# Kernel tuning notes

Hardware: AMD Instinct MI355X
Metric: run time of the kernel (lower is better)

## Reference

```python
import jax, jax.numpy as jnp
import numpy as np

N = 8192   # nodes per modality
D = 128    # hidden_channels
H = 2      # transformer heads
R = 15     # relations in HeteroConv (use_speaker='no')
E = 16384  # edges per relation
L = 2      # num_layers
# relation src/dst node-type ids: 0=audio, 1=text, 2=visual (dict order: a/v/t past, a/v/t future, a/v/t self, then cross)
SRC = np.array([0, 2, 1, 0, 2, 1, 0, 2, 1, 0, 0, 2, 2, 1, 1])
DST = np.array([0, 2, 1, 0, 2, 1, 0, 2, 1, 2, 1, 0, 1, 0, 2])


def setup_inputs() -> dict:
    key = jax.random.key(0)
    ks = jax.random.split(key, 18)
    f = lambda k, sh: jax.random.normal(k, sh, dtype=jnp.float32) * 0.05
    return {
        "x_audio": jax.random.normal(ks[0], (N, D), jnp.float32),
        "x_text": jax.random.normal(ks[1], (N, D), jnp.float32),
        "x_visual": jax.random.normal(ks[2], (N, D), jnp.float32),
        "edge_index": jax.random.randint(ks[3], (R, 2, E), 0, N, jnp.int32),
        "Wrel": f(ks[4], (L, R, D, D)),
        "brel": f(ks[5], (L, R, D)),
        "Wroot": f(ks[6], (L, R, D, D)),
        "Wq": f(ks[7], (D, H * D)), "bq": f(ks[8], (H * D,)),
        "Wk": f(ks[9], (D, H * D)), "bk": f(ks[10], (H * D,)),
        "Wv": f(ks[11], (D, H * D)), "bv": f(ks[12], (H * D,)),
        "Wskip": f(ks[13], (D, D)), "bskip": f(ks[14], (D,)),
        "gamma": jnp.ones((D,), jnp.float32),
        "beta": jnp.zeros((D,), jnp.float32),
    }


def reference(x_audio, x_text, x_visual, edge_index, Wrel, brel, Wroot,
              Wq, bq, Wk, bk, Wv, bv, Wskip, bskip, gamma, beta):
    src_t = jnp.asarray(SRC)
    dst_t = jnp.asarray(DST)
    x = jnp.stack([x_audio, x_text, x_visual])           # [3, N, D]
    src_idx = edge_index[:, 0]                            # [R, E]
    dst_idx = edge_index[:, 1]                            # [R, E]
    rel = jnp.arange(R)

    # --- HeteroConv of 15 GraphConvs (aggr='add' inside, 'mean' over the 5 relations per dst type) ---
    seg = (rel[:, None] * N + dst_idx).reshape(-1)        # per-relation segment ids
    for l in range(L):
        feats = jnp.take_along_axis(x[src_t], src_idx[:, :, None], axis=1)     # [R, E, D]
        msg = jax.ops.segment_sum(feats.reshape(R * E, D), seg,
                                  num_segments=R * N).reshape(R, N, D)          # scatter-add per relation
        out = (jnp.einsum('rnd,rde->rne', msg, Wrel[l]) + brel[l][:, None, :]
               + jnp.einsum('rnd,rde->rne', x[dst_t], Wroot[l]))                # lin_rel(agg) + lin_root(x_dst)
        x = jax.nn.relu(jnp.zeros_like(x).at[dst_t].add(out) / 5.0)            # mean over 5 relations per dst

    # --- hetero_to_homo: concat audio, text, visual (offsets 0, N, 2N) ---
    hx = x.reshape(3 * N, D)
    src_h = (src_t[:, None] * N + src_idx).reshape(-1)    # [R*E]
    dst_h = (dst_t[:, None] * N + dst_idx).reshape(-1)

    # --- TransformerConv (concat=False -> head mean, root skip) ---
    q = (hx @ Wq + bq).reshape(3 * N, H, D)
    k = (hx @ Wk + bk).reshape(3 * N, H, D)
    v = (hx @ Wv + bv).reshape(3 * N, H, D)
    logits = jnp.einsum('ehd,ehd->eh', q[dst_h], k[src_h]) / jnp.sqrt(jnp.float32(D))
    m = jax.ops.segment_max(logits, dst_h, num_segments=3 * N)
    p = jnp.exp(logits - m[dst_h])
    denom = jax.ops.segment_sum(p, dst_h, num_segments=3 * N)
    alpha = p / denom[dst_h]                              # segment softmax over incoming edges
    agg = jax.ops.segment_sum(alpha[:, :, None] * v[src_h], dst_h, num_segments=3 * N)  # [3N, H, D]
    out = agg.mean(axis=1) + hx @ Wskip + bskip

    # --- BatchNorm1d (training-mode batch stats) + leaky_relu ---
    mu = out.mean(axis=0)
    var = ((out - mu) ** 2).mean(axis=0)
    y = (out - mu) / jnp.sqrt(var + 1e-5) * gamma + beta
    y = jax.nn.leaky_relu(y)                              # negative_slope=0.01 (torch default)
    return y.reshape(3, N, D)                             # [audio, text, visual]
```

## Files before the change

kernel.cpp:

```cpp
#include <hip/hip_runtime.h>
#include <hip/hip_bf16.h>

#define NN 8192
#define DD 128
#define HH 2
#define RR 15
#define EE 16384
#define NLAYER 2
#define NMOD 3
#define TN (NMOD*NN)
#define NE (RR*EE)
#define NB (TN*5)
#define SCB (NB/256)

#define SRC_BITS 0x16818618u
#define DST_BITS 0x21198618u
__device__ __forceinline__ int srcOf(int r) { return (SRC_BITS >> (2 * r)) & 3; }
__device__ __forceinline__ int dstOf(int r) { return (DST_BITS >> (2 * r)) & 3; }

typedef __attribute__((ext_vector_type(8))) short bf16x8;
typedef __attribute__((ext_vector_type(4))) float f32x4;
typedef _Float16 h2 __attribute__((ext_vector_type(2)));

__device__ __forceinline__ unsigned short f2bf(float v) {
    union { float f; unsigned int u; } x; x.f = v;
    unsigned int r = (x.u + 0x7fffu + ((x.u >> 16) & 1u)) >> 16;
    return (unsigned short)r;
}
__device__ __forceinline__ float bf2f(unsigned int bits16) {
    return __uint_as_float(bits16 << 16);
}

__device__ __forceinline__ float dot8_f16(uint4 a, uint4 b, float acc) {
#if __has_builtin(__builtin_amdgcn_fdot2)
    acc = __builtin_amdgcn_fdot2(__builtin_bit_cast(h2, a.x), __builtin_bit_cast(h2, b.x), acc, false);
    acc = __builtin_amdgcn_fdot2(__builtin_bit_cast(h2, a.y), __builtin_bit_cast(h2, b.y), acc, false);
    acc = __builtin_amdgcn_fdot2(__builtin_bit_cast(h2, a.z), __builtin_bit_cast(h2, b.z), acc, false);
    acc = __builtin_amdgcn_fdot2(__builtin_bit_cast(h2, a.w), __builtin_bit_cast(h2, b.w), acc, false);
#else
    h2 av, bv;
    av = __builtin_bit_cast(h2, a.x); bv = __builtin_bit_cast(h2, b.x);
    acc += (float)av.x * (float)bv.x + (float)av.y * (float)bv.y;
    av = __builtin_bit_cast(h2, a.y); bv = __builtin_bit_cast(h2, b.y);
    acc += (float)av.x * (float)bv.x + (float)av.y * (float)bv.y;
    av = __builtin_bit_cast(h2, a.z); bv = __builtin_bit_cast(h2, b.z);
    acc += (float)av.x * (float)bv.x + (float)av.y * (float)bv.y;
    av = __builtin_bit_cast(h2, a.w); bv = __builtin_bit_cast(h2, b.w);
    acc += (float)av.x * (float)bv.x + (float)av.y * (float)bv.y;
#endif
    return acc;
}

__device__ __forceinline__ h2 h2shfl_xor(h2 a, int off) {
    return __builtin_bit_cast(h2, __shfl_xor(__builtin_bit_cast(int, a), off));
}

__global__ __launch_bounds__(256) void prep_all(
        const float* __restrict__ Wrel, const float* __restrict__ Wroot,
        const float* __restrict__ brel,
        const float* __restrict__ Wq, const float* __restrict__ Wk,
        const float* __restrict__ Wv, const float* __restrict__ Wskip,
        const float* __restrict__ xa, const float* __restrict__ xt,
        const float* __restrict__ xv,
        unsigned short* __restrict__ WcatT, float* __restrict__ bsum,
        unsigned short* __restrict__ WqT, unsigned short* __restrict__ WkT,
        unsigned short* __restrict__ WvT, unsigned short* __restrict__ WskipT,
        unsigned short* __restrict__ xb, int* __restrict__ cnt) {
    int y = blockIdx.y;
    int t = blockIdx.x * 256 + threadIdx.x;
    if (y < 36) {
        int mat = y / 6, j = y - mat * 6;
        int l = mat / 3, m = mat - l * 3;
        int k = t >> 7, oc = t & 127;
        unsigned short* W = WcatT + (size_t)mat * 128 * 768;
        if (j < 5) {
            int r = 3 * j;
            while (((DST_BITS >> (2 * r)) & 3) != (unsigned)m) r++;
            W[(size_t)oc * 768 + j * 128 + k] = f2bf(Wrel[(size_t)(l * RR + r) * 16384 + t]);
        } else {
            float s = 0.f;
            #pragma unroll
            for (int r = 0; r < RR; r++)
                if (((DST_BITS >> (2 * r)) & 3) == (unsigned)m) s += Wroot[(size_t)(l * RR + r) * 16384 + t];
            W[(size_t)oc * 768 + 640 + k] = f2bf(s);
            if (blockIdx.x == 0 && threadIdx.x < 128) {
                float b = 0.f;
                #pragma unroll
                for (int r = 0; r < RR; r++)
                    if (((DST_BITS >> (2 * r)) & 3) == (unsigned)m) b += brel[(l * RR + r) * 128 + threadIdx.x];
                bsum[mat * 128 + threadIdx.x] = b;
            }
        }
    } else if (y < 39) {
        int which = y - 36;
        const float* s = which == 0 ? Wq : which == 1 ? Wk : Wv;
        unsigned short* d = which == 0 ? WqT : which == 1 ? WkT : WvT;
        #pragma unroll
        for (int it = 0; it < 2; it++) {
            int tt = t + it * 16384;
            int k = tt >> 8, c = tt & 255;
            d[c * 128 + k] = f2bf(s[tt]);
        }
    } else if (y == 39) {
        int k = t >> 7, c = t & 127;
        WskipT[c * 128 + k] = f2bf(Wskip[t]);
    } else if (y == 40) {
        for (int i = t; i < NB + 256; i += 16384) cnt[i] = 0;
    } else {
        int m = y - 41;
        const float* s = m == 0 ? xa : m == 1 ? xt : xv;
        unsigned short* d = xb + (size_t)m * NN * DD;
        for (int i = t * 4; i < NN * DD; i += 16384 * 4) {
            float4 v = *(const float4*)(s + i);
            uint2 o;
            o.x = (unsigned)f2bf(v.x) | ((unsigned)f2bf(v.y) << 16);
            o.y = (unsigned)f2bf(v.z) | ((unsigned)f2bf(v.w) << 16);
            *(uint2*)(d + i) = o;
        }
    }
}

__global__ void count_edges(const int* __restrict__ edge, int* __restrict__ cnt) {
    int t = blockIdx.x * 256 + threadIdx.x;
    if (t >= NE) return;
    int r = t >> 14, e = t & (EE - 1);
    int dst = edge[r * 2 * EE + EE + e];
    atomicAdd(&cnt[(dstOf(r) * NN + dst) * 5 + r / 3], 1);
}

__global__ __launch_bounds__(256) void scan_reduce(const int* __restrict__ cnt,
                                                   int* __restrict__ part) {
    int t = threadIdx.x;
    int v = cnt[blockIdx.x * 256 + t];
    #pragma unroll
    for (int off = 32; off >= 1; off >>= 1) v += __shfl_xor(v, off);
    __shared__ int ws[4];
    if ((t & 63) == 0) ws[t >> 6] = v;
    __syncthreads();
    if (t == 0) part[blockIdx.x] = ws[0] + ws[1] + ws[2] + ws[3];
}

__global__ __launch_bounds__(512) void scan_mid(int* __restrict__ part, int* __restrict__ bs) {
    __shared__ int lds[512];
    int t = threadIdx.x;
    int v = (t < SCB) ? part[t] : 0;
    lds[t] = v;
    __syncthreads();
    for (int off = 1; off < 512; off <<= 1) {
        int u = (t >= off) ? lds[t - off] : 0;
        __syncthreads();
        lds[t] += u;
        __syncthreads();
    }
    if (t < SCB) part[t] = lds[t] - v;
    if (t == 0) bs[NB] = NE;
}

__global__ __launch_bounds__(256) void scan_final(const int* __restrict__ cnt,
                                                  const int* __restrict__ part,
                                                  int* __restrict__ bs,
                                                  int* __restrict__ cursor) {
    int t = threadIdx.x;
    int lane = t & 63, w = t >> 6;
    int i = blockIdx.x * 256 + t;
    int v = cnt[i];
    int inc = v;
    #pragma unroll
    for (int off = 1; off < 64; off <<= 1) {
        int u = __shfl_up(inc, off);
        if (lane >= off) inc += u;
    }
    __shared__ int wtot[4];
    if (lane == 63) wtot[w] = inc;
    __syncthreads();
    int wofs = 0;
    #pragma unroll
    for (int j = 0; j < 4; j++) if (j < w) wofs += wtot[j];
    int ex = part[blockIdx.x] + wofs + inc - v;
    bs[i] = ex;
    cursor[i] = ex;
}

__global__ void place_edges(const int* __restrict__ edge, int* __restrict__ cursor,
                            unsigned int* __restrict__ sorted) {
    int t = blockIdx.x * 256 + threadIdx.x;
    if (t >= NE) return;
    int r = t >> 14, e = t & (EE - 1);
    int src = edge[r * 2 * EE + e];
    int dst = edge[r * 2 * EE + EE + e];
    int pos = atomicAdd(&cursor[(dstOf(r) * NN + dst) * 5 + r / 3], 1);
    sorted[pos] = (unsigned int)(srcOf(r) * NN + src);
}

__global__ __launch_bounds__(256) void gather_msg(const unsigned short* __restrict__ x,
                                                  const unsigned int* __restrict__ sorted,
                                                  const int* __restrict__ bs,
                                                  unsigned short* __restrict__ msg) {
    int h = blockIdx.x * 4 + (threadIdx.x >> 6);
    int lane = threadIdx.x & 63;
    const unsigned int* x32 = (const unsigned int*)x;
    unsigned int* mrow = (unsigned int*)(msg + (size_t)h * 768);
    int base = h * 5;
    int st = bs[base];
    #pragma unroll
    for (int j = 0; j < 5; j++) {
        int nx = bs[base + j + 1];
        float a0 = 0.f, a1 = 0.f;
        for (int e = st; e < nx; e++) {
            unsigned int u = x32[(size_t)sorted[e] * 64 + lane];
            a0 += bf2f(u & 0xffffu);
            a1 += bf2f(u >> 16);
        }
        mrow[j * 64 + lane] = (unsigned)f2bf(a0) | ((unsigned)f2bf(a1) << 16);
        st = nx;
    }
    mrow[320 + lane] = x32[(size_t)h * 64 + lane];
}

__global__ __launch_bounds__(256) void layer_gemm(const unsigned short* __restrict__ msg,
                                                  const unsigned short* __restrict__ WcatT_l,
                                                  const float* __restrict__ bsum_l,
                                                  unsigned short* __restrict__ xnxt) {
    __shared__ unsigned short lds[24576];
    unsigned short* Alds = lds;
    unsigned short* Blds = lds + 8192;
    const int m = blockIdx.y;
    const int row0 = blockIdx.x * 64;
    const unsigned short* A = msg + ((size_t)m * NN + row0) * 768;
    const unsigned short* BT = WcatT_l + (size_t)m * 128 * 768;
    const int tid = threadIdx.x, lane = tid & 63, w = tid >> 6;
    const int lr = lane & 15, lk = lane >> 4;
    f32x4 acc[8];
    #pragma unroll
    for (int nj = 0; nj < 8; nj++) acc[nj] = (f32x4){0.f, 0.f, 0.f, 0.f};
    #pragma unroll 1
    for (int kc = 0; kc < 6; kc++) {
        __syncthreads();
        #pragma unroll
        for (int i = 0; i < 4; i++) {
            int c = i * 256 + tid;
            int row = c >> 4, k0 = (c & 15) << 3;
            uint4 va = *(const uint4*)(A + (size_t)row * 768 + kc * 128 + k0);
            *(uint4*)((char*)Alds + ((row * 256 + k0 * 2) ^ ((row & 7) << 4))) = va;
        }
        #pragma unroll
        for (int i = 0; i < 8; i++) {
            int c = i * 256 + tid;
            int row = c >> 4, k0 = (c & 15) << 3;
            uint4 vb = *(const uint4*)(BT + (size_t)row * 768 + kc * 128 + k0);
            *(uint4*)((char*)Blds + ((row * 256 + k0 * 2) ^ ((row & 7) << 4))) = vb;
        }
        __syncthreads();
        #pragma unroll
        for (int ks = 0; ks < 4; ks++) {
            int arow = w * 16 + lr;
            bf16x8 a = *(const bf16x8*)((char*)Alds + ((arow * 256 + (ks * 32 + lk * 8) * 2) ^ ((arow & 7) << 4)));
            bf16x8 b[8];
            #pragma unroll
            for (int nj = 0; nj < 8; nj++) {
                int brow = nj * 16 + lr;
                b[nj] = *(const bf16x8*)((char*)Blds + ((brow * 256 + (ks * 32 + lk * 8) * 2) ^ ((brow & 7) << 4)));
            }
            #pragma unroll
            for (int nj = 0; nj < 8; nj++)
                acc[nj] = __builtin_amdgcn_mfma_f32_16x16x32_bf16(a, b[nj], acc[nj], 0, 0, 0);
        }
    }
    __syncthreads();
    float* Clds = (float*)lds;
    #pragma unroll
    for (int nj = 0; nj < 8; nj++) {
        int col = nj * 16 + lr;
        float bb = bsum_l[m * 128 + col];
        #pragma unroll
        for (int r = 0; r < 4; r++) {
            int row = w * 16 + lk * 4 + r;
            float v = (acc[nj][r] + bb) * 0.2f;
            Clds[row * 128 + col] = v > 0.f ? v : 0.f;
        }
    }
    __syncthreads();
    unsigned short* X = xnxt + ((size_t)m * NN + row0) * 128;
    #pragma unroll
    for (int i = 0; i < 4; i++) {
        int c = i * 256 + tid;
        int row = c >> 4, c0 = (c & 15) * 8;
        float4 fa = *(const float4*)(Clds + row * 128 + c0);
        float4 fb = *(const float4*)(Clds + row * 128 + c0 + 4);
        uint4 pk;
        pk.x = (unsigned)f2bf(fa.x) | ((unsigned)f2bf(fa.y) << 16);
        pk.y = (unsigned)f2bf(fa.z) | ((unsigned)f2bf(fa.w) << 16);
        pk.z = (unsigned)f2bf(fb.x) | ((unsigned)f2bf(fb.y) << 16);
        pk.w = (unsigned)f2bf(fb.z) | ((unsigned)f2bf(fb.w) << 16);
        *(uint4*)(X + (size_t)row * 128 + c0) = pk;
    }
}

template<int MODE>
__device__ __forceinline__ void gemm_tile(const unsigned short* __restrict__ A,
                                          const unsigned short* __restrict__ BT,
                                          const float* __restrict__ bias,
                                          void* __restrict__ Cout,
                                          int ldc, int colofs, int row0,
                                          unsigned short* lds, float oscale = 1.f) {
    unsigned short* Alds = lds;
    unsigned short* Blds = lds + 16384;
    const int tid = threadIdx.x;
    const int lane = tid & 63;
    const int w = tid >> 6;
    #pragma unroll
    for (int i = 0; i < 8; i++) {
        int c = i * 256 + tid;
        int row = c >> 4;
        int k0 = (c & 15) << 3;
        uint4 va = *(const uint4*)(A + (size_t)(row0 + row) * 128 + k0);
        *(uint4*)((char*)Alds + (((row * 256 + k0 * 2)) ^ ((row & 7) << 4))) = va;
        uint4 vb = *(const uint4*)(BT + (size_t)row * 128 + k0);
        *(uint4*)((char*)Blds + (((row * 256 + k0 * 2)) ^ ((row & 7) << 4))) = vb;
    }
    __syncthreads();
    f32x4 acc[2][8];
    #pragma unroll
    for (int mi = 0; mi < 2; mi++)
        #pragma unroll
        for (int nj = 0; nj < 8; nj++) acc[mi][nj] = (f32x4){0.f, 0.f, 0.f, 0.f};
    const int lr = lane & 15, lk = lane >> 4;
    #pragma unroll
    for (int ks = 0; ks < 4; ks++) {
        bf16x8 a[2], b[8];
        #pragma unroll
        for (int mi = 0; mi < 2; mi++) {
            int row = w * 32 + mi * 16 + lr;
            a[mi] = *(const bf16x8*)((char*)Alds + ((row * 256 + (ks * 32 + lk * 8) * 2) ^ ((row & 7) << 4)));
        }
        #pragma unroll
        for (int nj = 0; nj < 8; nj++) {
            int row = nj * 16 + lr;
            b[nj] = *(const bf16x8*)((char*)Blds + ((row * 256 + (ks * 32 + lk * 8) * 2) ^ ((row & 7) << 4)));
        }
        #pragma unroll
        for (int mi = 0; mi < 2; mi++)
            #pragma unroll
            for (int nj = 0; nj < 8; nj++)
                acc[mi][nj] = __builtin_amdgcn_mfma_f32_16x16x32_bf16(a[mi], b[nj], acc[mi][nj], 0, 0, 0);
    }
    __syncthreads();
    float* Clds = (float*)lds;
    #pragma unroll
    for (int mi = 0; mi < 2; mi++) {
        #pragma unroll
        for (int nj = 0; nj < 8; nj++) {
            int ccl = nj * 16 + lr;
            float bb = bias ? bias[ccl] : 0.f;
            #pragma unroll
            for (int r = 0; r < 4; r++) {
                int row = w * 32 + mi * 16 + lk * 4 + r;
                Clds[row * 128 + ccl] = acc[mi][nj][r] + bb;
            }
        }
    }
    __syncthreads();
    #pragma unroll
    for (int p = 0; p < 8; p++) {
        int row = p * 16 + (tid >> 4);
        int c0 = (tid & 15) * 8;
        float4 fa = *(const float4*)(Clds + row * 128 + c0);
        float4 fb = *(const float4*)(Clds + row * 128 + c0 + 4);
        if (MODE == 3) {
            unsigned r0 = __builtin_bit_cast(unsigned, __builtin_amdgcn_cvt_pkrtz(fa.x * oscale, fa.y * oscale));
            unsigned r1 = __builtin_bit_cast(unsigned, __builtin_amdgcn_cvt_pkrtz(fa.z * oscale, fa.w * oscale));
            unsigned r2 = __builtin_bit_cast(unsigned, __builtin_amdgcn_cvt_pkrtz(fb.x * oscale, fb.y * oscale));
            unsigned r3 = __builtin_bit_cast(unsigned, __builtin_amdgcn_cvt_pkrtz(fb.z * oscale, fb.w * oscale));
            uint4 pk = {r0, r1, r2, r3};
            *(uint4*)((unsigned short*)Cout + (size_t)(row0 + row) * ldc + colofs + c0) = pk;
        } else {
            float* Cf = (float*)Cout;
            *(float4*)(Cf + (size_t)(row0 + row) * ldc + colofs + c0) = fa;
            *(float4*)(Cf + (size_t)(row0 + row) * ldc + colofs + c0 + 4) = fb;
        }
    }
}

__global__ __launch_bounds__(256) void qkvskip_gemm(const unsigned short* __restrict__ xbf,
                                                    const unsigned short* __restrict__ WqT,
                                                    const unsigned short* __restrict__ WkT,
                                                    const unsigned short* __restrict__ WvT,
                                                    const unsigned short* __restrict__ WskipT,
                                                    const float* __restrict__ bq,
                                                    const float* __restrict__ bk,
                                                    const float* __restrict__ bv,
                                                    const float* __restrict__ bskip,
                                                    unsigned short* __restrict__ qb,
                                                    unsigned short* __restrict__ kb,
                                                    unsigned short* __restrict__ vb,
                                                    float* __restrict__ out) {
    __shared__ unsigned short lds[2 * 16384];
    int y = blockIdx.y;
    if (y < 6) {
        int which = y >> 1, half = y & 1;
        const unsigned short* BT = (which == 0 ? WqT : which == 1 ? WkT : WvT) + half * 16384;
        const float* bias = (which == 0 ? bq : which == 1 ? bk : bv) + half * 128;
        unsigned short* C = (which == 0 ? qb : which == 1 ? kb : vb);
        float os = (which == 0) ? 0.08838834764831845f : 1.f;
        gemm_tile<3>(xbf, BT, bias, C, 256, half * 128, blockIdx.x * 128, lds, os);
    } else {
        gemm_tile<0>(xbf, WskipT, bskip, out, 128, 0, blockIdx.x * 128, lds);
    }
}

__global__ __launch_bounds__(256) void attn_fused(const unsigned short* __restrict__ qb,
                                                  const unsigned short* __restrict__ kb,
                                                  const unsigned short* __restrict__ vb,
                                                  const unsigned int* __restrict__ sorted,
                                                  const int* __restrict__ bs,
                                                  float* __restrict__ out) {
    int node = blockIdx.x * 4 + (threadIdx.x >> 6);
    int lane = threadIdx.x & 63;
    int g = lane >> 4, p = lane & 15;
    uint4 q0 = *(const uint4*)(qb + (size_t)node * 256 + p * 8);
    uint4 q1 = *(const uint4*)(qb + (size_t)node * 256 + 128 + p * 8);
    float s0 = 0.f, s1 = 0.f;
    h2 a0h[4], a1h[4];
    #pragma unroll
    for (int jj = 0; jj < 4; jj++) { a0h[jj] = (h2){0, 0}; a1h[jj] = (h2){0, 0}; }
    int st = bs[node * 5], en = bs[node * 5 + 5];
    int idx = st + g;
    unsigned int vcur = (idx < en) ? sorted[idx] : 0u;
    for (int base = st; base < en; base += 4) {
        unsigned int vnext = (idx + 4 < en) ? sorted[idx + 4] : 0u;
        bool valid = idx < en;
        const unsigned short* krow = kb + (size_t)vcur * 256;
        const unsigned short* vrow = vb + (size_t)vcur * 256;
        uint4 k0r = *(const uint4*)(krow + p * 8);
        uint4 k1r = *(const uint4*)(krow + 128 + p * 8);
        uint4 v0r = *(const uint4*)(vrow + p * 8);
        uint4 v1r = *(const uint4*)(vrow + 128 + p * 8);
        float d0 = dot8_f16(q0, k0r, 0.f);
        float d1 = dot8_f16(q1, k1r, 0.f);
        #pragma unroll
        for (int off = 8; off >= 1; off >>= 1) {
            d0 += __shfl_xor(d0, off);
            d1 += __shfl_xor(d1, off);
        }
        float p0 = valid ? __expf(d0) : 0.f;
        float p1 = valid ? __expf(d1) : 0.f;
        s0 += p0; s1 += p1;
        h2 ph0 = (h2){(_Float16)p0, (_Float16)p0};
        h2 ph1 = (h2){(_Float16)p1, (_Float16)p1};
        a0h[0] += ph0 * __builtin_bit_cast(h2, v0r.x);
        a0h[1] += ph0 * __builtin_bit_cast(h2, v0r.y);
        a0h[2] += ph0 * __builtin_bit_cast(h2, v0r.z);
        a0h[3] += ph0 * __builtin_bit_cast(h2, v0r.w);
        a1h[0] += ph1 * __builtin_bit_cast(h2, v1r.x);
        a1h[1] += ph1 * __builtin_bit_cast(h2, v1r.y);
        a1h[2] += ph1 * __builtin_bit_cast(h2, v1r.z);
        a1h[3] += ph1 * __builtin_bit_cast(h2, v1r.w);
        vcur = vnext;
        idx += 4;
    }
    #pragma unroll
    for (int off = 32; off >= 16; off >>= 1) {
        s0 += __shfl_xor(s0, off);
        s1 += __shfl_xor(s1, off);
        #pragma unroll
        for (int jj = 0; jj < 4; jj++) {
            a0h[jj] += h2shfl_xor(a0h[jj], off);
            a1h[jj] += h2shfl_xor(a1h[jj], off);
        }
    }
    if (g == 0) {
        float inv0 = (s0 > 0.f) ? 0.5f / s0 : 0.f;
        float inv1 = (s1 > 0.f) ? 0.5f / s1 : 0.f;
        float a0[8], a1[8];
        #pragma unroll
        for (int jj = 0; jj < 4; jj++) {
            a0[2 * jj] = (float)a0h[jj].x; a0[2 * jj + 1] = (float)a0h[jj].y;
            a1[2 * jj] = (float)a1h[jj].x; a1[2 * jj + 1] = (float)a1h[jj].y;
        }
        float* op = out + (size_t)node * 128 + p * 8;
        float4 ska = *(const float4*)op;
        float4 skb = *(const float4*)(op + 4);
        float4 ra, rb;
        ra.x = a0[0] * inv0 + a1[0] * inv1 + ska.x;
        ra.y = a0[1] * inv0 + a1[1] * inv1 + ska.y;
        ra.z = a0[2] * inv0 + a1[2] * inv1 + ska.z;
        ra.w = a0[3] * inv0 + a1[3] * inv1 + ska.w;
        rb.x = a0[4] * inv0 + a1[4] * inv1 + skb.x;
        rb.y = a0[5] * inv0 + a1[5] * inv1 + skb.y;
        rb.z = a0[6] * inv0 + a1[6] * inv1 + skb.z;
        rb.w = a0[7] * inv0 + a1[7] * inv1 + skb.w;
        *(float4*)op = ra;
        *(float4*)(op + 4) = rb;
    }
}

__global__ void colstats(const float* __restrict__ outb, float* __restrict__ stats) {
    int col = threadIdx.x & 127;
    int sub = threadIdx.x >> 7;
    float s = 0.f, ss = 0.f;
    for (int row = blockIdx.x * 2 + sub; row < TN; row += gridDim.x * 2) {
        float vv = outb[(size_t)row * DD + col];
        s += vv;
        ss += vv * vv;
    }
    __shared__ float red[2][256];
    red[0][threadIdx.x] = s;
    red[1][threadIdx.x] = ss;
    __syncthreads();
    if (sub == 0) {
        s  += red[0][threadIdx.x + 128];
        ss += red[1][threadIdx.x + 128];
        atomicAdd(&stats[col], s);
        atomicAdd(&stats[DD + col], ss);
    }
}

__global__ void ln_act(float* __restrict__ outb, const float* __restrict__ stats,
                       const float* __restrict__ gamma, const float* __restrict__ beta) {
    int i = (blockIdx.x * 256 + threadIdx.x) * 4;
    if (i >= TN * DD) return;
    int col = i & 127;
    float4 v = *(const float4*)(outb + i);
    float o[4] = {v.x, v.y, v.z, v.w};
    #pragma unroll
    for (int j = 0; j < 4; j++) {
        int c = col + j;
        float mu = stats[c] * (1.f / TN);
        float var = stats[DD + c] * (1.f / TN) - mu * mu;
        float inv = rsqrtf(var + 1e-5f);
        float vv = (o[j] - mu) * inv * gamma[c] + beta[c];
        o[j] = vv > 0.f ? vv : 0.01f * vv;
    }
    float4 res = {o[0], o[1], o[2], o[3]};
    *(float4*)(outb + i) = res;
}

extern "C" void kernel_launch(void* const* d_in, const int* in_sizes, int n_in,
                              void* d_out, int out_size, void* d_ws, size_t ws_size,
                              hipStream_t stream) {
    const float* x_audio = (const float*)d_in[0];
    const float* x_text  = (const float*)d_in[1];
    const float* x_vis   = (const float*)d_in[2];
    const int*   edge    = (const int*)d_in[3];
    const float* Wrel    = (const float*)d_in[4];
    const float* brel    = (const float*)d_in[5];
    const float* Wroot   = (const float*)d_in[6];
    const float* Wq      = (const float*)d_in[7];
    const float* bq      = (const float*)d_in[8];
    const float* Wk      = (const float*)d_in[9];
    const float* bk      = (const float*)d_in[10];
    const float* Wv      = (const float*)d_in[11];
    const float* bv      = (const float*)d_in[12];
    const float* Wskip   = (const float*)d_in[13];
    const float* bskip   = (const float*)d_in[14];
    const float* gamma   = (const float*)d_in[15];
    const float* beta    = (const float*)d_in[16];
    float* out = (float*)d_out;

    char* p = (char*)d_ws;
    unsigned short* xbfA = (unsigned short*)p; p += (size_t)TN * 128 * 2;
    unsigned short* xbfB = (unsigned short*)p; p += (size_t)TN * 128 * 2;
    unsigned short* msg = (unsigned short*)p; p += (size_t)TN * 768 * 2;
    unsigned short* qb = msg;
    unsigned short* kb = msg + (size_t)TN * 256;
    unsigned short* vb = msg + (size_t)2 * TN * 256;
    unsigned short* WcatT = (unsigned short*)p; p += (size_t)6 * 128 * 768 * 2;
    float* brelSum = (float*)p; p += 6 * 128 * 4;
    unsigned short* WqT = (unsigned short*)p; p += 256 * 128 * 2;
    unsigned short* WkT = (unsigned short*)p; p += 256 * 128 * 2;
    unsigned short* WvT = (unsigned short*)p; p += 256 * 128 * 2;
    unsigned short* WskipT = (unsigned short*)p; p += 128 * 128 * 2;
    unsigned int* sorted = (unsigned int*)p; p += (size_t)NE * 4;
    int* bs = (int*)p; p += (size_t)(NB + 4) * 4;
    int* cursor = (int*)p; p += (size_t)NB * 4;
    int* cnt = (int*)p; p += (size_t)NB * 4;
    float* stats = (float*)p; p += 256 * 4;
    int* part = (int*)p; p += SCB * 4;
    size_t needed = (size_t)(p - (char*)d_ws);
    if (ws_size < needed) return;

    prep_all<<<dim3(64, 44), 256, 0, stream>>>(Wrel, Wroot, brel, Wq, Wk, Wv, Wskip,
                                               x_audio, x_text, x_vis,
                                               WcatT, brelSum,
                                               WqT, WkT, WvT, WskipT, xbfA, cnt);

    count_edges<<<NE / 256, 256, 0, stream>>>(edge, cnt);
    scan_reduce<<<SCB, 256, 0, stream>>>(cnt, part);
    scan_mid<<<1, 512, 0, stream>>>(part, bs);
    scan_final<<<SCB, 256, 0, stream>>>(cnt, part, bs, cursor);
    place_edges<<<NE / 256, 256, 0, stream>>>(edge, cursor, sorted);

    unsigned short* xcur = xbfA;
    unsigned short* xnxt = xbfB;
    for (int l = 0; l < NLAYER; ++l) {
        gather_msg<<<TN / 4, 256, 0, stream>>>(xcur, sorted, bs, msg);
        layer_gemm<<<dim3(NN / 64, NMOD), 256, 0, stream>>>(
            msg, WcatT + (size_t)l * NMOD * 128 * 768, brelSum + l * NMOD * 128, xnxt);
        unsigned short* t = xcur; xcur = xnxt; xnxt = t;
    }

    qkvskip_gemm<<<dim3(TN / 128, 7), 256, 0, stream>>>(xcur, WqT, WkT, WvT, WskipT,
                                                        bq, bk, bv, bskip, qb, kb, vb, out);
    attn_fused<<<TN / 4, 256, 0, stream>>>(qb, kb, vb, sorted, bs, out);

    colstats<<<384, 256, 0, stream>>>(out, stats);
    ln_act<<<(TN * DD) / 1024, 256, 0, stream>>>(out, stats, gamma, beta);
}
```

Baseline: 234.3 us.

## Interleave K/V rows for attention gather and halve layer GEMM row tile

K and V are now written into one interleaved buffer (512 bf16 per node), so each edge in the attention kernel fetches its K and V data from one contiguous 1 KB row. Each lane now covers 16 channels and 8 edges are processed per iteration instead of 4, which doubles the loads in flight per wave. Separately, the relation GEMM tile shrinks from 64 to 32 rows with a 2x2 wave split, doubling the block count to improve occupancy and load balance. The cost is more redundant loads of the B (weight) tile across blocks and higher register pressure in the attention kernel.

New measurement: 257.2 us. 1.1x slower.

```diff
diff --git a/kernel.cpp b/kernel.cpp
--- a/kernel.cpp
+++ b/kernel.cpp
@@ -221,23 +221,24 @@
                                                   const unsigned short* __restrict__ WcatT_l,
                                                   const float* __restrict__ bsum_l,
                                                   unsigned short* __restrict__ xnxt) {
-    __shared__ unsigned short lds[24576];
+    __shared__ unsigned short lds[20480];
     unsigned short* Alds = lds;
-    unsigned short* Blds = lds + 8192;
+    unsigned short* Blds = lds + 4096;
     const int m = blockIdx.y;
-    const int row0 = blockIdx.x * 64;
+    const int row0 = blockIdx.x * 32;
     const unsigned short* A = msg + ((size_t)m * NN + row0) * 768;
     const unsigned short* BT = WcatT_l + (size_t)m * 128 * 768;
     const int tid = threadIdx.x, lane = tid & 63, w = tid >> 6;
+    const int wr = w >> 1, wc = w & 1;
     const int lr = lane & 15, lk = lane >> 4;
-    f32x4 acc[8];
-    #pragma unroll
-    for (int nj = 0; nj < 8; nj++) acc[nj] = (f32x4){0.f, 0.f, 0.f, 0.f};
+    f32x4 acc[4];
+    #pragma unroll
+    for (int nj = 0; nj < 4; nj++) acc[nj] = (f32x4){0.f, 0.f, 0.f, 0.f};
     #pragma unroll 1
     for (int kc = 0; kc < 6; kc++) {
         __syncthreads();
         #pragma unroll
-        for (int i = 0; i < 4; i++) {
+        for (int i = 0; i < 2; i++) {
             int c = i * 256 + tid;
             int row = c >> 4, k0 = (c & 15) << 3;
             uint4 va = *(const uint4*)(A + (size_t)row * 768 + kc * 128 + k0);
@@ -253,28 +254,28 @@
         __syncthreads();
         #pragma unroll
         for (int ks = 0; ks < 4; ks++) {
-            int arow = w * 16 + lr;
+            int arow = wr * 16 + lr;
             bf16x8 a = *(const bf16x8*)((char*)Alds + ((arow * 256 + (ks * 32 + lk * 8) * 2) ^ ((arow & 7) << 4)));
-            bf16x8 b[8];
+            bf16x8 b[4];
             #pragma unroll
-            for (int nj = 0; nj < 8; nj++) {
-                int brow = nj * 16 + lr;
+            for (int nj = 0; nj < 4; nj++) {
+                int brow = wc * 64 + nj * 16 + lr;
                 b[nj] = *(const bf16x8*)((char*)Blds + ((brow * 256 + (ks * 32 + lk * 8) * 2) ^ ((brow & 7) << 4)));
             }
             #pragma unroll
-            for (int nj = 0; nj < 8; nj++)
+            for (int nj = 0; nj < 4; nj++)
                 acc[nj] = __builtin_amdgcn_mfma_f32_16x16x32_bf16(a, b[nj], acc[nj], 0, 0, 0);
         }
     }
     __syncthreads();
     float* Clds = (float*)lds;
     #pragma unroll
-    for (int nj = 0; nj < 8; nj++) {
-        int col = nj * 16 + lr;
+    for (int nj = 0; nj < 4; nj++) {
+        int col = wc * 64 + nj * 16 + lr;
         float bb = bsum_l[m * 128 + col];
         #pragma unroll
         for (int r = 0; r < 4; r++) {
-            int row = w * 16 + lk * 4 + r;
+            int row = wr * 16 + lk * 4 + r;
             float v = (acc[nj][r] + bb) * 0.2f;
             Clds[row * 128 + col] = v > 0.f ? v : 0.f;
         }
@@ -282,7 +283,7 @@
     __syncthreads();
     unsigned short* X = xnxt + ((size_t)m * NN + row0) * 128;
     #pragma unroll
-    for (int i = 0; i < 4; i++) {
+    for (int i = 0; i < 2; i++) {
         int c = i * 256 + tid;
         int row = c >> 4, c0 = (c & 15) * 8;
         float4 fa = *(const float4*)(Clds + row * 128 + c0);
@@ -391,54 +392,63 @@
                                                     const float* __restrict__ bv,
                                                     const float* __restrict__ bskip,
                                                     unsigned short* __restrict__ qb,
-                                                    unsigned short* __restrict__ kb,
-                                                    unsigned short* __restrict__ vb,
+                                                    unsigned short* __restrict__ kvb,
                                                     float* __restrict__ out) {
     __shared__ unsigned short lds[2 * 16384];
     int y = blockIdx.y;
-    if (y < 6) {
-        int which = y >> 1, half = y & 1;
-        const unsigned short* BT = (which == 0 ? WqT : which == 1 ? WkT : WvT) + half * 16384;
-        const float* bias = (which == 0 ? bq : which == 1 ? bk : bv) + half * 128;
-        unsigned short* C = (which == 0 ? qb : which == 1 ? kb : vb);
-        float os = (which == 0) ? 0.08838834764831845f : 1.f;
-        gemm_tile<3>(xbf, BT, bias, C, 256, half * 128, blockIdx.x * 128, lds, os);
+    if (y < 2) {
+        int half = y & 1;
+        gemm_tile<3>(xbf, WqT + half * 16384, bq + half * 128, qb, 256, half * 128,
+                     blockIdx.x * 128, lds, 0.08838834764831845f);
+    } else if (y < 4) {
+        int half = y & 1;
+        gemm_tile<3>(xbf, WkT + half * 16384, bk + half * 128, kvb, 512, half * 128,
+                     blockIdx.x * 128, lds, 1.f);
+    } else if (y < 6) {
+        int half = y & 1;
+        gemm_tile<3>(xbf, WvT + half * 16384, bv + half * 128, kvb, 512, 256 + half * 128,
+                     blockIdx.x * 128, lds, 1.f);
     } else {
         gemm_tile<0>(xbf, WskipT, bskip, out, 128, 0, blockIdx.x * 128, lds);
     }
 }
 
 __global__ __launch_bounds__(256) void attn_fused(const unsigned short* __restrict__ qb,
-                                                  const unsigned short* __restrict__ kb,
-                                                  const unsigned short* __restrict__ vb,
+                                                  const unsigned short* __restrict__ kvb,
                                                   const unsigned int* __restrict__ sorted,
                                                   const int* __restrict__ bs,
                                                   float* __restrict__ out) {
     int node = blockIdx.x * 4 + (threadIdx.x >> 6);
     int lane = threadIdx.x & 63;
-    int g = lane >> 4, p = lane & 15;
-    uint4 q0 = *(const uint4*)(qb + (size_t)node * 256 + p * 8);
-    uint4 q1 = *(const uint4*)(qb + (size_t)node * 256 + 128 + p * 8);
+    int g = lane >> 3, p = lane & 7;
+    const unsigned short* qrow = qb + (size_t)node * 256 + p * 16;
+    uint4 q0a = *(const uint4*)(qrow);
+    uint4 q0b = *(const uint4*)(qrow + 8);
+    uint4 q1a = *(const uint4*)(qrow + 128);
+    uint4 q1b = *(const uint4*)(qrow + 136);
     float s0 = 0.f, s1 = 0.f;
-    h2 a0h[4], a1h[4];
-    #pragma unroll
-    for (int jj = 0; jj < 4; jj++) { a0h[jj] = (h2){0, 0}; a1h[jj] = (h2){0, 0}; }
+    h2 a0h[8], a1h[8];
+    #pragma unroll
+    for (int jj = 0; jj < 8; jj++) { a0h[jj] = (h2){0, 0}; a1h[jj] = (h2){0, 0}; }
     int st = bs[node * 5], en = bs[node * 5 + 5];
     int idx = st + g;
     unsigned int vcur = (idx < en) ? sorted[idx] : 0u;
-    for (int base = st; base < en; base += 4) {
-        unsigned int vnext = (idx + 4 < en) ? sorted[idx + 4] : 0u;
+    for (int base = st; base < en; base += 8) {
+        unsigned int vnext = (idx + 8 < en) ? sorted[idx + 8] : 0u;
         bool valid = idx < en;
-        const unsigned short* krow = kb + (size_t)vcur * 256;
-        const unsigned short* vrow = vb + (size_t)vcur * 256;
-        uint4 k0r = *(const uint4*)(krow + p * 8);
-        uint4 k1r = *(const uint4*)(krow + 128 + p * 8);
-        uint4 v0r = *(const uint4*)(vrow + p * 8);
-        uint4 v1r = *(const uint4*)(vrow + 128 + p * 8);
-        float d0 = dot8_f16(q0, k0r, 0.f);
-        float d1 = dot8_f16(q1, k1r, 0.f);
-        #pragma unroll
-        for (int off = 8; off >= 1; off >>= 1) {
+        const unsigned short* kv = kvb + (size_t)vcur * 512 + p * 16;
+        uint4 k0a = *(const uint4*)(kv);
+        uint4 k0b = *(const uint4*)(kv + 8);
+        uint4 k1a = *(const uint4*)(kv + 128);
+        uint4 k1b = *(const uint4*)(kv + 136);
+        uint4 v0a = *(const uint4*)(kv + 256);
+        uint4 v0b = *(const uint4*)(kv + 264);
+        uint4 v1a = *(const uint4*)(kv + 384);
+        uint4 v1b = *(const uint4*)(kv + 392);
+        float d0 = dot8_f16(q0b, k0b, dot8_f16(q0a, k0a, 0.f));
+        float d1 = dot8_f16(q1b, k1b, dot8_f16(q1a, k1a, 0.f));
+        #pragma unroll
+        for (int off = 4; off >= 1; off >>= 1) {
             d0 += __shfl_xor(d0, off);
             d1 += __shfl_xor(d1, off);
         }
@@ -447,23 +457,31 @@
         s0 += p0; s1 += p1;
         h2 ph0 = (h2){(_Float16)p0, (_Float16)p0};
         h2 ph1 = (h2){(_Float16)p1, (_Float16)p1};
-        a0h[0] += ph0 * __builtin_bit_cast(h2, v0r.x);
-        a0h[1] += ph0 * __builtin_bit_cast(h2, v0r.y);
-        a0h[2] += ph0 * __builtin_bit_cast(h2, v0r.z);
-        a0h[3] += ph0 * __builtin_bit_cast(h2, v0r.w);
-        a1h[0] += ph1 * __builtin_bit_cast(h2, v1r.x);
-        a1h[1] += ph1 * __builtin_bit_cast(h2, v1r.y);
-        a1h[2] += ph1 * __builtin_bit_cast(h2, v1r.z);
-        a1h[3] += ph1 * __builtin_bit_cast(h2, v1r.w);
+        a0h[0] += ph0 * __builtin_bit_cast(h2, v0a.x);
+        a0h[1] += ph0 * __builtin_bit_cast(h2, v0a.y);
+        a0h[2] += ph0 * __builtin_bit_cast(h2, v0a.z);
+        a0h[3] += ph0 * __builtin_bit_cast(h2, v0a.w);
+        a0h[4] += ph0 * __builtin_bit_cast(h2, v0b.x);
+        a0h[5] += ph0 * __builtin_bit_cast(h2, v0b.y);
+        a0h[6] += ph0 * __builtin_bit_cast(h2, v0b.z);
+        a0h[7] += ph0 * __builtin_bit_cast(h2, v0b.w);
+        a1h[0] += ph1 * __builtin_bit_cast(h2, v1a.x);
+        a1h[1] += ph1 * __builtin_bit_cast(h2, v1a.y);
+        a1h[2] += ph1 * __builtin_bit_cast(h2, v1a.z);
+        a1h[3] += ph1 * __builtin_bit_cast(h2, v1a.w);
+        a1h[4] += ph1 * __builtin_bit_cast(h2, v1b.x);
+        a1h[5] += ph1 * __builtin_bit_cast(h2, v1b.y);
+        a1h[6] += ph1 * __builtin_bit_cast(h2, v1b.z);
+        a1h[7] += ph1 * __builtin_bit_cast(h2, v1b.w);
         vcur = vnext;
-        idx += 4;
-    }
-    #pragma unroll
-    for (int off = 32; off >= 16; off >>= 1) {
+        idx += 8;
+    }
+    #pragma unroll
+    for (int off = 32; off >= 8; off >>= 1) {
         s0 += __shfl_xor(s0, off);
         s1 += __shfl_xor(s1, off);
         #pragma unroll
-        for (int jj = 0; jj < 4; jj++) {
+        for (int jj = 0; jj < 8; jj++) {
             a0h[jj] += h2shfl_xor(a0h[jj], off);
             a1h[jj] += h2shfl_xor(a1h[jj], off);
         }
@@ -471,26 +489,17 @@
     if (g == 0) {
         float inv0 = (s0 > 0.f) ? 0.5f / s0 : 0.f;
         float inv1 = (s1 > 0.f) ? 0.5f / s1 : 0.f;
-        float a0[8], a1[8];
-        #pragma unroll
-        for (int jj = 0; jj < 4; jj++) {
-            a0[2 * jj] = (float)a0h[jj].x; a0[2 * jj + 1] = (float)a0h[jj].y;
-            a1[2 * jj] = (float)a1h[jj].x; a1[2 * jj + 1] = (float)a1h[jj].y;
-        }
-        float* op = out + (size_t)node * 128 + p * 8;
-        float4 ska = *(const float4*)op;
-        float4 skb = *(const float4*)(op + 4);
-        float4 ra, rb;
-        ra.x = a0[0] * inv0 + a1[0] * inv1 + ska.x;
-        ra.y = a0[1] * inv0 + a1[1] * inv1 + ska.y;
-        ra.z = a0[2] * inv0 + a1[2] * inv1 + ska.z;
-        ra.w = a0[3] * inv0 + a1[3] * inv1 + ska.w;
-        rb.x = a0[4] * inv0 + a1[4] * inv1 + skb.x;
-        rb.y = a0[5] * inv0 + a1[5] * inv1 + skb.y;
-        rb.z = a0[6] * inv0 + a1[6] * inv1 + skb.z;
-        rb.w = a0[7] * inv0 + a1[7] * inv1 + skb.w;
-        *(float4*)op = ra;
-        *(float4*)(op + 4) = rb;
+        float* op = out + (size_t)node * 128 + p * 16;
+        #pragma unroll
+        for (int half = 0; half < 4; half++) {
+            float4 sk = *(const float4*)(op + half * 4);
+            float4 r;
+            r.x = (float)a0h[half * 2].x     * inv0 + (float)a1h[half * 2].x     * inv1 + sk.x;
+            r.y = (float)a0h[half * 2].y     * inv0 + (float)a1h[half * 2].y     * inv1 + sk.y;
+            r.z = (float)a0h[half * 2 + 1].x * inv0 + (float)a1h[half * 2 + 1].x * inv1 + sk.z;
+            r.w = (float)a0h[half * 2 + 1].y * inv0 + (float)a1h[half * 2 + 1].y * inv1 + sk.w;
+            *(float4*)(op + half * 4) = r;
+        }
     }
 }
 
@@ -561,9 +570,8 @@
     unsigned short* xbfA = (unsigned short*)p; p += (size_t)TN * 128 * 2;
     unsigned short* xbfB = (unsigned short*)p; p += (size_t)TN * 128 * 2;
     unsigned short* msg = (unsigned short*)p; p += (size_t)TN * 768 * 2;
-    unsigned short* qb = msg;
-    unsigned short* kb = msg + (size_t)TN * 256;
-    unsigned short* vb = msg + (size_t)2 * TN * 256;
+    unsigned short* qb  = msg;
+    unsigned short* kvb = msg + (size_t)TN * 256;
     unsigned short* WcatT = (unsigned short*)p; p += (size_t)6 * 128 * 768 * 2;
     float* brelSum = (float*)p; p += 6 * 128 * 4;
     unsigned short* WqT = (unsigned short*)p; p += 256 * 128 * 2;
@@ -594,14 +602,14 @@
     unsigned short* xnxt = xbfB;
     for (int l = 0; l < NLAYER; ++l) {
         gather_msg<<<TN / 4, 256, 0, stream>>>(xcur, sorted, bs, msg);
-        layer_gemm<<<dim3(NN / 64, NMOD), 256, 0, stream>>>(
+        layer_gemm<<<dim3(NN / 32, NMOD), 256, 0, stream>>>(
             msg, WcatT + (size_t)l * NMOD * 128 * 768, brelSum + l * NMOD * 128, xnxt);
         unsigned short* t = xcur; xcur = xnxt; xnxt = t;
     }
 
     qkvskip_gemm<<<dim3(TN / 128, 7), 256, 0, stream>>>(xcur, WqT, WkT, WvT, WskipT,
-                                                        bq, bk, bv, bskip, qb, kb, vb, out);
-    attn_fused<<<TN / 4, 256, 0, stream>>>(qb, kb, vb, sorted, bs, out);
+                                                        bq, bk, bv, bskip, qb, kvb, out);
+    attn_fused<<<TN / 4, 256, 0, stream>>>(qb, kvb, sorted, bs, out);
 
     colstats<<<384, 256, 0, stream>>>(out, stats);
     ln_act<<<(TN * DD) / 1024, 256, 0, stream>>>(out, stats, gamma, beta);
```
